# Optimization experiments

Measured on AMD Instinct MI355X. Metric: run time of the kernel, lower is better.

The kernel has to match this reference:

```python
import jax, jax.numpy as jnp
import numpy as np

EPS_LN = 1e-5
EPS_BN = 1e-5
NUM_HEADS = 8


def _gelu(x):
    return jax.nn.gelu(x, approximate=False)


def _ln(x, w, b):
    # LayerNorm over last (channel) dim, eps=1e-5 (torch default)
    mu = jnp.mean(x, axis=-1, keepdims=True)
    var = jnp.mean((x - mu) ** 2, axis=-1, keepdims=True)
    return (x - mu) / jnp.sqrt(var + EPS_LN) * w + b


def _bn(x, g, b):
    # eval-mode BatchNorm2d on NCHW with running_mean=0, running_var=1
    scale = g * (1.0 + EPS_BN) ** -0.5
    return x * scale[None, :, None, None] + b[None, :, None, None]


def _conv1x1(x, w):
    # x: [B,C,H,W], w: [O,C]
    return jnp.einsum('bchw,oc->bohw', x, w)


def _unfold3(x, r):
    # nn.Unfold(kernel=3, dilation=r, padding=r): gather 3x3 dilated neighborhoods
    B, C, H, W = x.shape
    xp = jnp.pad(x, ((0, 0), (0, 0), (r, r), (r, r)))
    pats = [xp[:, :, i * r:i * r + H, j * r:j * r + W] for i in range(3) for j in range(3)]
    return jnp.stack(pats, axis=2)  # [B,C,9,H,W]


def _atrous_attn(q, k, v, num_heads, r):
    # per-pixel local attention: q [B,C,H,W] attends to 9 dilated neighbors of k/v
    B, C, H, W = q.shape
    hd = C // num_heads
    scale = hd ** -0.5
    qh = q.reshape(B, num_heads, hd, H, W)
    kp = _unfold3(k, r).reshape(B, num_heads, hd, 9, H, W)
    attn = jax.nn.softmax(jnp.einsum('bnchw,bnckhw->bnkhw', qh, kp) * scale, axis=2)
    vp = _unfold3(v, r).reshape(B, num_heads, hd, 9, H, W)
    out = jnp.einsum('bnkhw,bnckhw->bnchw', attn, vp)
    return out.reshape(B, C, H, W).transpose(0, 2, 3, 1)  # [B,H,W,C]


def _window_attn(x_bhwc, qkv_w, proj_w, proj_b, num_heads, r):
    xc = x_bhwc.transpose(0, 3, 1, 2)
    C = xc.shape[1]
    qkv = _conv1x1(xc, qkv_w)  # [B,3C,H,W], order q|k|v
    out = _atrous_attn(qkv[:, :C], qkv[:, C:2 * C], qkv[:, 2 * C:], num_heads, r)
    return jnp.einsum('bhwc,oc->bhwo', out, proj_w) + proj_b


def _mlp(x_bhwc, c1_w, c1_b, bn1_g, bn1_b, dw_w, dw_b, bn2_g, bn2_b, c2_w, c2_b, bn3_g, bn3_b):
    xc = x_bhwc.transpose(0, 3, 1, 2)
    h = _bn(_gelu(_conv1x1(xc, c1_w) + c1_b[None, :, None, None]), bn1_g, bn1_b)
    dw = jax.lax.conv_general_dilated(h, dw_w, (1, 1), 'SAME',
                                      feature_group_count=h.shape[1],
                                      dimension_numbers=('NCHW', 'OIHW', 'NCHW'))
    dw = dw + dw_b[None, :, None, None]
    h = _bn(_gelu(dw + h), bn2_g, bn2_b)
    out = _bn(_conv1x1(h, c2_w) + c2_b[None, :, None, None], bn3_g, bn3_b)
    return out.transpose(0, 2, 3, 1)


def reference(x, ln1_w, ln1_b, ln2_w, ln2_b,
              qkv1_w, proj1_w, proj1_b, qkv2_w, proj2_w, proj2_b, qkv3_w, proj3_w, proj3_b,
              tc_conv_w, tc_conv_b, tc_bn1_g, tc_bn1_b, tc_pool_w, tc_bn2_g, tc_bn2_b,
              tc_trans_w, tc_trans_b, tc_bn3_g, tc_bn3_b,
              mlp_c1_w, mlp_c1_b, mlp_bn1_g, mlp_bn1_b, mlp_dw_w, mlp_dw_b,
              mlp_bn2_g, mlp_bn2_b, mlp_c2_w, mlp_c2_b, mlp_bn3_g, mlp_bn3_b):
    tx = x.transpose(0, 2, 3, 1)  # [B,H,W,C]
    n1 = _ln(tx, ln1_w, ln1_b)
    t1 = tx + _window_attn(n1, qkv1_w, proj1_w, proj1_b, NUM_HEADS, 1)
    t2 = tx + _window_attn(n1, qkv2_w, proj2_w, proj2_b, NUM_HEADS, 2)
    t3 = tx + _window_attn(n1, qkv3_w, proj3_w, proj3_b, NUM_HEADS, 3)
    # Trans_conv: ASPP-style fusion
    xc1 = jax.nn.relu(_bn(_conv1x1(x, tc_conv_w) + tc_conv_b[None, :, None, None], tc_bn1_g, tc_bn1_b))
    pool = jnp.mean(x, axis=(2, 3), keepdims=True)
    pool = jax.nn.relu(_bn(_conv1x1(pool, tc_pool_w), tc_bn2_g, tc_bn2_b))
    pool = jnp.broadcast_to(pool, x.shape)  # bilinear upsample of a 1x1 map == broadcast
    cat = jnp.concatenate([xc1, t1.transpose(0, 3, 1, 2), t2.transpose(0, 3, 1, 2),
                           t3.transpose(0, 3, 1, 2), pool], axis=1)  # [B,5C,H,W]
    tr = jax.nn.relu(_bn(_conv1x1(cat, tc_trans_w) + tc_trans_b[None, :, None, None],
                         tc_bn3_g, tc_bn3_b)).transpose(0, 2, 3, 1)  # [B,H,W,C]
    tr = tr + _mlp(_ln(tr, ln2_w, ln2_b), mlp_c1_w, mlp_c1_b, mlp_bn1_g, mlp_bn1_b,
                   mlp_dw_w, mlp_dw_b, mlp_bn2_g, mlp_bn2_b, mlp_c2_w, mlp_c2_b,
                   mlp_bn3_g, mlp_bn3_b)
    return tr.transpose(0, 3, 1, 2)  # [B,C,H,W]


def setup_inputs():
    key = jax.random.key(0)
    B, C, H, W = 4, 256, 64, 64
    HID = 4 * C
    ks = iter(jax.random.split(key, 64))

    def nrm(shape, scale=0.02):
        return jax.random.normal(next(ks), shape, dtype=jnp.float32) * scale

    inp = {
        'x': jax.random.normal(next(ks), (B, C, H, W), dtype=jnp.float32),
        'ln1_w': jnp.ones((C,), jnp.float32), 'ln1_b': jnp.zeros((C,), jnp.float32),
        'ln2_w': jnp.ones((C,), jnp.float32), 'ln2_b': jnp.zeros((C,), jnp.float32),
    }
    for i in (1, 2, 3):
        inp[f'qkv{i}_w'] = nrm((3 * C, C))
        inp[f'proj{i}_w'] = nrm((C, C))
        inp[f'proj{i}_b'] = jnp.zeros((C,), jnp.float32)
    inp.update(
        tc_conv_w=nrm((C, C)), tc_conv_b=jnp.zeros((C,), jnp.float32),
        tc_bn1_g=jnp.ones((C,), jnp.float32), tc_bn1_b=jnp.zeros((C,), jnp.float32),
        tc_pool_w=nrm((C, C)),
        tc_bn2_g=jnp.ones((C,), jnp.float32), tc_bn2_b=jnp.zeros((C,), jnp.float32),
        tc_trans_w=nrm((C, 5 * C)), tc_trans_b=jnp.zeros((C,), jnp.float32),
        tc_bn3_g=jnp.ones((C,), jnp.float32), tc_bn3_b=jnp.zeros((C,), jnp.float32),
        mlp_c1_w=nrm((HID, C)), mlp_c1_b=jnp.zeros((HID,), jnp.float32),
        mlp_bn1_g=jnp.ones((HID,), jnp.float32), mlp_bn1_b=jnp.zeros((HID,), jnp.float32),
        mlp_dw_w=nrm((HID, 1, 3, 3), 0.1), mlp_dw_b=jnp.zeros((HID,), jnp.float32),
        mlp_bn2_g=jnp.ones((HID,), jnp.float32), mlp_bn2_b=jnp.zeros((HID,), jnp.float32),
        mlp_c2_w=nrm((C, HID)), mlp_c2_b=jnp.zeros((C,), jnp.float32),
        mlp_bn3_g=jnp.ones((C,), jnp.float32), mlp_bn3_b=jnp.zeros((C,), jnp.float32),
    )
    return inp
```

## Files before the change

kernel.cpp:

```cpp
#include <hip/hip_runtime.h>

#define N_PIX 16384
#define CDIM  256
#define HIDD  1024
#define BNS   0.9999950000374997f

typedef __attribute__((ext_vector_type(8))) short  short8;
typedef __attribute__((ext_vector_type(4))) float  f32x4;
typedef __attribute__((ext_vector_type(4))) int    int4v;
typedef __attribute__((ext_vector_type(2))) int    int2v;

__device__ __forceinline__ float b2f(unsigned short u){
  unsigned int x = ((unsigned int)u) << 16; float f;
  __builtin_memcpy(&f, &x, 4); return f;
}
__device__ __forceinline__ unsigned short f2b(float f){
  unsigned int x; __builtin_memcpy(&x, &f, 4);
  unsigned int r = (x + 0x7fffu + ((x >> 16) & 1u)) >> 16;
  return (unsigned short)r;
}
__device__ __forceinline__ float geluf(float x){
  return 0.5f * x * (1.0f + erff(x * 0.70710678118654752f));
}

typedef const __attribute__((address_space(1))) unsigned int* gas_t;
typedef __attribute__((address_space(3))) unsigned int*       las_t;
__device__ __forceinline__ void gload16(const void* g, void* l){
  __builtin_amdgcn_global_load_lds((gas_t)g, (las_t)l, 16, 0, 0);
}

__global__ __launch_bounds__(256) void k_cvt_all(
    const float* __restrict__ s0, const float* __restrict__ s1, const float* __restrict__ s2,
    const float* __restrict__ s3, const float* __restrict__ s4, const float* __restrict__ s5,
    const float* __restrict__ s6, const float* __restrict__ s7, const float* __restrict__ s8,
    const float* __restrict__ s9, unsigned short* __restrict__ wb){
  const float* srcs[10] = {s0,s1,s2,s3,s4,s5,s6,s7,s8,s9};
  const int n[10]   = {196608,196608,196608,65536,65536,65536,65536,327680,262144,262144};
  const int off[10] = {0,196608,393216,589824,655360,720896,786432,851968,1179648,1441792};
  int seg = blockIdx.y;
  int i = (blockIdx.x * 256 + threadIdx.x) * 8;
  if (i >= n[seg]) return;
  const float* src = srcs[seg];
  unsigned short* dst = wb + off[seg];
  f32x4 a = *(const f32x4*)(src + i);
  f32x4 b = *(const f32x4*)(src + i + 4);
  unsigned short o[8];
  #pragma unroll
  for (int j = 0; j < 4; ++j){ o[j] = f2b(a[j]); o[4 + j] = f2b(b[j]); }
  *(int4v*)(dst + i) = *(int4v*)o;
}

__global__ __launch_bounds__(256) void k_dwwT(const float* __restrict__ dww,
                                              unsigned short* __restrict__ dwwT,
                                              float* __restrict__ pm){
  int i = blockIdx.x * 256 + threadIdx.x;
  if (i < 1024) pm[i] = 0.0f;
  if (i >= 9216) return;
  int kk = i >> 10, c = i & 1023;
  dwwT[i] = f2b(dww[c * 9 + kk]);
}

__global__ __launch_bounds__(256) void k_transpose(const float* __restrict__ x,
                                                   unsigned short* __restrict__ xpm,
                                                   float* __restrict__ xpm32,
                                                   float* __restrict__ pm){
  __shared__ __align__(16) float tile[64][65];
  int b = blockIdx.z, c0 = blockIdx.y * 64, p0 = blockIdx.x * 64;
  int t = threadIdx.x;
  int r = t >> 3, k = t & 7;
  float psum[2];
  for (int s = 0; s < 2; ++s){
    int rr = r + s * 32;
    const float* src = x + (((size_t)(b * CDIM + c0 + rr)) << 12) + p0 + k * 8;
    f32x4 a = *(const f32x4*)src;
    f32x4 c = *(const f32x4*)(src + 4);
    psum[s] = a[0] + a[1] + a[2] + a[3] + c[0] + c[1] + c[2] + c[3];
    #pragma unroll
    for (int j = 0; j < 4; ++j){ tile[rr][k * 8 + j] = a[j]; tile[rr][k * 8 + 4 + j] = c[j]; }
  }
  #pragma unroll
  for (int s = 0; s < 2; ++s){
    float v = psum[s];
    v += __shfl_xor(v, 1); v += __shfl_xor(v, 2); v += __shfl_xor(v, 4);
    if ((t & 7) == 0) atomicAdd(&pm[b * 256 + c0 + r + s * 32], v);
  }
  __syncthreads();
  for (int s = 0; s < 2; ++s){
    int pr = r + s * 32;
    float tf[8];
    unsigned short tb[8];
    #pragma unroll
    for (int j = 0; j < 8; ++j){ tf[j] = tile[k * 8 + j][pr]; tb[j] = f2b(tf[j]); }
    size_t rowoff = ((size_t)(b * 4096 + p0 + pr)) << 8;
    *(int4v*)(xpm + rowoff + c0 + k * 8) = *(int4v*)tb;
    *(f32x4*)(xpm32 + rowoff + c0 + k * 8)     = *(f32x4*)&tf[0];
    *(f32x4*)(xpm32 + rowoff + c0 + k * 8 + 4) = *(f32x4*)&tf[4];
  }
}

template<typename IT>
__global__ __launch_bounds__(256) void k_ln(const IT* __restrict__ in,
    const float* __restrict__ w, const float* __restrict__ bia,
    unsigned short* __restrict__ out){
  int row  = blockIdx.x * 4 + (threadIdx.x >> 6);
  int lane = threadIdx.x & 63;
  float v[4];
  const IT* p = in + (size_t)row * CDIM + lane * 4;
  if constexpr (sizeof(IT) == 2){
    int2v d = *(const int2v*)p;
    unsigned short tmp[4]; __builtin_memcpy(tmp, &d, 8);
    #pragma unroll
    for (int j = 0; j < 4; ++j) v[j] = b2f(tmp[j]);
  } else {
    f32x4 d = *(const f32x4*)p;
    #pragma unroll
    for (int j = 0; j < 4; ++j) v[j] = d[j];
  }
  float s  = v[0] + v[1] + v[2] + v[3];
  float s2 = v[0]*v[0] + v[1]*v[1] + v[2]*v[2] + v[3]*v[3];
  #pragma unroll
  for (int m = 1; m < 64; m <<= 1){
    s  += __shfl_xor(s,  m);
    s2 += __shfl_xor(s2, m);
  }
  float mu   = s * (1.0f / 256.0f);
  float var  = s2 * (1.0f / 256.0f) - mu * mu;
  float rstd = rsqrtf(var + 1e-5f);
  unsigned short o[4];
  #pragma unroll
  for (int j = 0; j < 4; ++j){
    int c = lane * 4 + j;
    o[j] = f2b((v[j] - mu) * rstd * w[c] + bia[c]);
  }
  *(int2v*)(out + (size_t)row * CDIM + lane * 4) = *(int2v*)o;
}

template<int MODE, int BM>
__global__ __launch_bounds__(256) void k_gemm(
    const unsigned short* __restrict__ A, const unsigned short* __restrict__ Bw,
    int K, int Nout, int ldb, void* __restrict__ outp,
    const float* __restrict__ bias,
    const float* __restrict__ bng,
    const float* __restrict__ bnb,
    const float* __restrict__ auxf,
    int catoff)
{
  constexpr int NI = BM / 32;
  __shared__ __align__(16) unsigned short As[2][BM * 32];
  __shared__ __align__(16) unsigned short Bs[2][128 * 32];
  int t = threadIdx.x;
  int m0 = blockIdx.y * BM, n0 = blockIdx.x * 128;
  int lane = t & 63;
  int w  = __builtin_amdgcn_readfirstlane(t >> 6);
  int wm = w >> 1, wn = w & 1;
  int lr = lane & 15, kb = lane >> 4;
  const bool doA = (w * 16 < BM);

  f32x4 acc[NI][4];
  f32x4 z = {0.f, 0.f, 0.f, 0.f};
  #pragma unroll
  for (int i = 0; i < NI; ++i)
    #pragma unroll
    for (int j = 0; j < 4; ++j) acc[i][j] = z;

  int srow = lane >> 2;
  int schunk = (((lane & 3) ^ ((lane >> 3) & 3))) * 8;
  const unsigned short* gA  = A  + (size_t)(m0 + w * 16 + srow) * K   + schunk;
  const unsigned short* gB0 = Bw + (size_t)(n0 + w * 16 + srow) * ldb + schunk;
  const unsigned short* gB1 = Bw + (size_t)(n0 + 64 + w * 16 + srow) * ldb + schunk;
  int kbx = (kb ^ ((lr >> 1) & 3)) * 8;

  const int nt = K >> 5;
  if (doA) gload16(gA, As[0] + w * 512);
  gload16(gB0, Bs[0] + w * 512);
  gload16(gB1, Bs[0] + 2048 + w * 512);

  for (int tt = 0; tt < nt; ++tt){
    int cur = tt & 1;
    if (tt + 1 < nt){
      int k1 = (tt + 1) << 5;
      if (doA) gload16(gA + k1, As[cur ^ 1] + w * 512);
      gload16(gB0 + k1, Bs[cur ^ 1] + w * 512);
      gload16(gB1 + k1, Bs[cur ^ 1] + 2048 + w * 512);
      if (doA) asm volatile("s_waitcnt vmcnt(3)" ::: "memory");
      else     asm volatile("s_waitcnt vmcnt(2)" ::: "memory");
    } else {
      asm volatile("s_waitcnt vmcnt(0)" ::: "memory");
    }
    __builtin_amdgcn_s_barrier();
    short8 af[NI], bf_[4];
    #pragma unroll
    for (int i = 0; i < NI; ++i)
      af [i] = *(const short8*)&As[cur][(wm * (BM / 2) + i * 16 + lr) * 32 + kbx];
    #pragma unroll
    for (int j = 0; j < 4; ++j)
      bf_[j] = *(const short8*)&Bs[cur][(wn * 64 + j * 16 + lr) * 32 + kbx];
    #pragma unroll
    for (int i = 0; i < NI; ++i)
      #pragma unroll
      for (int j = 0; j < 4; ++j)
        acc[i][j] = __builtin_amdgcn_mfma_f32_16x16x32_bf16(af[i], bf_[j], acc[i][j], 0, 0, 0);
    asm volatile("s_waitcnt lgkmcnt(0)" ::: "memory");
    __builtin_amdgcn_sched_barrier(0);
    __builtin_amdgcn_s_barrier();
  }

  #pragma unroll
  for (int i = 0; i < NI; ++i){
    int rowb = m0 + wm * (BM / 2) + i * 16 + kb * 4;
    #pragma unroll
    for (int j = 0; j < 4; ++j){
      int col = n0 + wn * 64 + j * 16 + lr;
      #pragma unroll
      for (int rr = 0; rr < 4; ++rr){
        int row = rowb + rr;
        float v = acc[i][j][rr];
        if constexpr (MODE == 0){
          ((unsigned short*)outp)[(size_t)row * Nout + col] = f2b(v);
        } else if constexpr (MODE == 3){
          v += bias[col] + auxf[((row >> 12) << 8) + col];
          v = v * (bng[col] * BNS) + bnb[col];
          v = fmaxf(v, 0.0f);
          ((float*)outp)[(size_t)row * CDIM + col] = v;
        } else if constexpr (MODE == 4){
          v = geluf(v + bias[col]);
          v = v * (bng[col] * BNS) + bnb[col];
          ((unsigned short*)outp)[(size_t)row * HIDD + col] = f2b(v);
        } else {
          v = (v + bias[col]) * (bng[col] * BNS) + bnb[col];
          v += auxf[(size_t)row * CDIM + col];
          int b = row >> 12, hw = row & 4095;
          ((float*)outp)[(((size_t)(b * CDIM + col)) << 12) + hw] = v;
        }
      }
    }
  }
}

struct GrpArgs {
  const unsigned short* A[4];
  const unsigned short* B[4];
  const float* bias[4];
  int lda[4];
  int catoff[4];
};

__global__ __launch_bounds__(256) void k_gemm_grp(GrpArgs ga,
    const float* __restrict__ xpm32, const float* __restrict__ bng,
    const float* __restrict__ bnb, unsigned short* __restrict__ CAT)
{
  __shared__ __align__(16) unsigned short As[2][64 * 32];
  __shared__ __align__(16) unsigned short Bs[2][128 * 32];
  int t = threadIdx.x;
  int g  = blockIdx.x >> 1;
  int n0 = (blockIdx.x & 1) * 128;
  int m0 = blockIdx.y * 64;
  const unsigned short* A  = ga.A[g];
  const unsigned short* Bw = ga.B[g];
  const float* bias = ga.bias[g];
  int lda = ga.lda[g];
  int catoff = ga.catoff[g];

  int lane = t & 63;
  int w  = __builtin_amdgcn_readfirstlane(t >> 6);
  int wm = w >> 1, wn = w & 1;
  int lr = lane & 15, kb = lane >> 4;

  f32x4 acc[2][4];
  f32x4 z = {0.f, 0.f, 0.f, 0.f};
  #pragma unroll
  for (int i = 0; i < 2; ++i)
    #pragma unroll
    for (int j = 0; j < 4; ++j) acc[i][j] = z;

  int srow = lane >> 2;
  int schunk = (((lane & 3) ^ ((lane >> 3) & 3))) * 8;
  const unsigned short* gA  = A  + (size_t)(m0 + w * 16 + srow) * lda + schunk;
  const unsigned short* gB0 = Bw + (size_t)(n0 + w * 16 + srow) * 256 + schunk;
  const unsigned short* gB1 = Bw + (size_t)(n0 + 64 + w * 16 + srow) * 256 + schunk;
  int kbx = (kb ^ ((lr >> 1) & 3)) * 8;

  gload16(gA,  As[0] + w * 512);
  gload16(gB0, Bs[0] + w * 512);
  gload16(gB1, Bs[0] + 2048 + w * 512);

  for (int tt = 0; tt < 8; ++tt){
    int cur = tt & 1;
    if (tt + 1 < 8){
      int k1 = (tt + 1) << 5;
      gload16(gA  + k1, As[cur ^ 1] + w * 512);
      gload16(gB0 + k1, Bs[cur ^ 1] + w * 512);
      gload16(gB1 + k1, Bs[cur ^ 1] + 2048 + w * 512);
      asm volatile("s_waitcnt vmcnt(3)" ::: "memory");
    } else {
      asm volatile("s_waitcnt vmcnt(0)" ::: "memory");
    }
    __builtin_amdgcn_s_barrier();
    short8 af[2], bf_[4];
    #pragma unroll
    for (int i = 0; i < 2; ++i)
      af [i] = *(const short8*)&As[cur][(wm * 32 + i * 16 + lr) * 32 + kbx];
    #pragma unroll
    for (int j = 0; j < 4; ++j)
      bf_[j] = *(const short8*)&Bs[cur][(wn * 64 + j * 16 + lr) * 32 + kbx];
    #pragma unroll
    for (int i = 0; i < 2; ++i)
      #pragma unroll
      for (int j = 0; j < 4; ++j)
        acc[i][j] = __builtin_amdgcn_mfma_f32_16x16x32_bf16(af[i], bf_[j], acc[i][j], 0, 0, 0);
    asm volatile("s_waitcnt lgkmcnt(0)" ::: "memory");
    __builtin_amdgcn_sched_barrier(0);
    __builtin_amdgcn_s_barrier();
  }

  #pragma unroll
  for (int i = 0; i < 2; ++i){
    int rowb = m0 + wm * 32 + i * 16 + kb * 4;
    #pragma unroll
    for (int j = 0; j < 4; ++j){
      int col = n0 + wn * 64 + j * 16 + lr;
      #pragma unroll
      for (int rr = 0; rr < 4; ++rr){
        int row = rowb + rr;
        float v = acc[i][j][rr];
        if (g == 3){
          v = (v + bias[col]) * (bng[col] * BNS) + bnb[col];
          v = fmaxf(v, 0.0f);
        } else {
          v += bias[col] + xpm32[(size_t)row * CDIM + col];
        }
        CAT[(size_t)row * HIDD + catoff + col] = f2b(v);
      }
    }
  }
}

__global__ __launch_bounds__(256) void k_attn3(const unsigned short* __restrict__ QKV3,
                                               unsigned short* __restrict__ F3){
  int grp = blockIdx.x >> 10;
  int r = grp + 1;
  int t = (blockIdx.x & 1023) * 256 + threadIdx.x;
  int half = t & 1, head = (t >> 1) & 7, pix = t >> 4;
  int hw = pix & 4095, h = hw >> 6, w = hw & 63;
  const unsigned short* base = QKV3 + (size_t)pix * 2304 + grp * 768 + head * 32 + half * 16;

  float q[16];
  #pragma unroll
  for (int c8 = 0; c8 < 2; ++c8){
    int4v d = *(const int4v*)(base + c8 * 8);
    unsigned short tmp[8]; __builtin_memcpy(tmp, &d, 16);
    #pragma unroll
    for (int j = 0; j < 8; ++j) q[c8 * 8 + j] = b2f(tmp[j]);
  }
  float logit[9];
  #pragma unroll
  for (int jj = 0; jj < 9; ++jj){
    int dh = (jj / 3 - 1) * r, dw = (jj % 3 - 1) * r;
    int hh = h + dh, ww = w + dw;
    float d = 0.0f;
    if (hh >= 0 && hh < 64 && ww >= 0 && ww < 64){
      const unsigned short* kr = base + (dh * 64 + dw) * 2304 + 256;
      #pragma unroll
      for (int c8 = 0; c8 < 2; ++c8){
        int4v dd = *(const int4v*)(kr + c8 * 8);
        unsigned short tmp[8]; __builtin_memcpy(tmp, &dd, 16);
        #pragma unroll
        for (int j = 0; j < 8; ++j) d += q[c8 * 8 + j] * b2f(tmp[j]);
      }
    }
    d += __shfl_xor(d, 1);
    logit[jj] = d * 0.17677669529663687f;
  }
  float m = logit[0];
  #pragma unroll
  for (int jj = 1; jj < 9; ++jj) m = fmaxf(m, logit[jj]);
  float p[9], s = 0.0f;
  #pragma unroll
  for (int jj = 0; jj < 9; ++jj){ p[jj] = __expf(logit[jj] - m); s += p[jj]; }
  float inv = 1.0f / s;
  float o[16];
  #pragma unroll
  for (int j = 0; j < 16; ++j) o[j] = 0.0f;
  #pragma unroll
  for (int jj = 0; jj < 9; ++jj){
    int dh = (jj / 3 - 1) * r, dw = (jj % 3 - 1) * r;
    int hh = h + dh, ww = w + dw;
    if (hh >= 0 && hh < 64 && ww >= 0 && ww < 64){
      float pj = p[jj] * inv;
      const unsigned short* vr = base + (dh * 64 + dw) * 2304 + 512;
      #pragma unroll
      for (int c8 = 0; c8 < 2; ++c8){
        int4v dd = *(const int4v*)(vr + c8 * 8);
        unsigned short tmp[8]; __builtin_memcpy(tmp, &dd, 16);
        #pragma unroll
        for (int j = 0; j < 8; ++j) o[c8 * 8 + j] += pj * b2f(tmp[j]);
      }
    }
  }
  unsigned short ob[16];
  #pragma unroll
  for (int j = 0; j < 16; ++j) ob[j] = f2b(o[j]);
  unsigned short* op = F3 + (size_t)pix * 768 + grp * 256 + head * 32 + half * 16;
  *(int4v*)(op)     = *(int4v*)&ob[0];
  *(int4v*)(op + 8) = *(int4v*)&ob[8];
}

__global__ __launch_bounds__(256) void k_dwconv(const unsigned short* __restrict__ H,
    const unsigned short* __restrict__ dwwT, const float* __restrict__ dwb,
    const float* __restrict__ g, const float* __restrict__ bb,
    unsigned short* __restrict__ H2){
  int t = blockIdx.x * 256 + threadIdx.x;
  int chunk = t & 127, pix = t >> 7;
  int hw = pix & 4095, h = hw >> 6, w = hw & 63;
  int c0 = chunk * 8;
  float acc[8], hc[8];
  {
    int4v dd = *(const int4v*)(H + (size_t)pix * HIDD + c0);
    unsigned short tmp[8]; __builtin_memcpy(tmp, &dd, 16);
    #pragma unroll
    for (int j = 0; j < 8; ++j){ hc[j] = b2f(tmp[j]); acc[j] = 0.0f; }
  }
  #pragma unroll
  for (int di = -1; di <= 1; ++di)
    #pragma unroll
    for (int dj = -1; dj <= 1; ++dj){
      int hh = h + di, ww = w + dj;
      if (hh < 0 || hh >= 64 || ww < 0 || ww >= 64) continue;
      int kk = (di + 1) * 3 + (dj + 1);
      int4v dd = *(const int4v*)(H + ((size_t)(pix + di * 64 + dj)) * HIDD + c0);
      int4v wv = *(const int4v*)(dwwT + kk * 1024 + c0);
      unsigned short tmp[8], wt[8];
      __builtin_memcpy(tmp, &dd, 16);
      __builtin_memcpy(wt,  &wv, 16);
      #pragma unroll
      for (int j = 0; j < 8; ++j) acc[j] += b2f(wt[j]) * b2f(tmp[j]);
    }
  f32x4 bv0 = *(const f32x4*)(dwb + c0), bv1 = *(const f32x4*)(dwb + c0 + 4);
  f32x4 gv0 = *(const f32x4*)(g   + c0), gv1 = *(const f32x4*)(g   + c0 + 4);
  f32x4 cv0 = *(const f32x4*)(bb  + c0), cv1 = *(const f32x4*)(bb  + c0 + 4);
  float bvv[8], gvv[8], cvv[8];
  #pragma unroll
  for (int j = 0; j < 4; ++j){
    bvv[j] = bv0[j]; bvv[4 + j] = bv1[j];
    gvv[j] = gv0[j]; gvv[4 + j] = gv1[j];
    cvv[j] = cv0[j]; cvv[4 + j] = cv1[j];
  }
  unsigned short ob[8];
  #pragma unroll
  for (int j = 0; j < 8; ++j){
    float v = acc[j] + bvv[j] + hc[j];
    v = geluf(v);
    v = v * (gvv[j] * BNS) + cvv[j];
    ob[j] = f2b(v);
  }
  *(int4v*)(H2 + (size_t)pix * HIDD + c0) = *(int4v*)ob;
}

__global__ __launch_bounds__(256) void k_poolfb(const float* __restrict__ pm,
    const float* __restrict__ pw, const float* __restrict__ g,
    const float* __restrict__ bb, const float* __restrict__ tw,
    float* __restrict__ pb){
  int b = blockIdx.x, o = threadIdx.x;
  __shared__ float v[256];
  __shared__ float pfs[256];
  v[o] = pm[b * 256 + o] * (1.0f / 4096.0f);
  __syncthreads();
  float acc = 0.0f;
  const float* wr = pw + (size_t)o * 256;
  for (int c = 0; c < 256; ++c) acc += v[c] * wr[c];
  float val = acc * (g[o] * BNS) + bb[o];
  pfs[o] = fmaxf(val, 0.0f);
  __syncthreads();
  float acc2 = 0.0f;
  const float* tr = tw + (size_t)o * 1280 + 1024;
  for (int c = 0; c < 256; ++c) acc2 += pfs[c] * tr[c];
  pb[b * 256 + o] = acc2;
}

extern "C" void kernel_launch(void* const* d_in, const int* in_sizes, int n_in,
                              void* d_out, int out_size, void* d_ws, size_t ws_size,
                              hipStream_t stream){
  const float* x     = (const float*)d_in[0];
  const float* ln1w  = (const float*)d_in[1];
  const float* ln1b  = (const float*)d_in[2];
  const float* ln2w  = (const float*)d_in[3];
  const float* ln2b  = (const float*)d_in[4];
  const float* qkvw[3]  = {(const float*)d_in[5], (const float*)d_in[8],  (const float*)d_in[11]};
  const float* projw[3] = {(const float*)d_in[6], (const float*)d_in[9],  (const float*)d_in[12]};
  const float* projb[3] = {(const float*)d_in[7], (const float*)d_in[10], (const float*)d_in[13]};
  const float* tcw   = (const float*)d_in[14];
  const float* tcb   = (const float*)d_in[15];
  const float* bn1g  = (const float*)d_in[16];
  const float* bn1b  = (const float*)d_in[17];
  const float* poolw = (const float*)d_in[18];
  const float* bn2g  = (const float*)d_in[19];
  const float* bn2b  = (const float*)d_in[20];
  const float* trw   = (const float*)d_in[21];
  const float* trb   = (const float*)d_in[22];
  const float* bn3g  = (const float*)d_in[23];
  const float* bn3b  = (const float*)d_in[24];
  const float* c1w   = (const float*)d_in[25];
  const float* c1b   = (const float*)d_in[26];
  const float* mbn1g = (const float*)d_in[27];
  const float* mbn1b = (const float*)d_in[28];
  const float* dww   = (const float*)d_in[29];
  const float* dwb   = (const float*)d_in[30];
  const float* mbn2g = (const float*)d_in[31];
  const float* mbn2b = (const float*)d_in[32];
  const float* c2w   = (const float*)d_in[33];
  const float* c2b   = (const float*)d_in[34];
  const float* mbn3g = (const float*)d_in[35];
  const float* mbn3b = (const float*)d_in[36];

  char* ws = (char*)d_ws;
  unsigned short* Xpm = (unsigned short*)(ws);
  unsigned short* N1  = (unsigned short*)(ws + 8388608);
  unsigned short* CAT = (unsigned short*)(ws + 16777216);
  float*          TR  = (float*)        (ws + 50331648);
  float*          Xpm32 = TR;
  unsigned short* H   = (unsigned short*)(ws + 67108864);
  unsigned short* H2  = (unsigned short*)(ws + 100663296);
  unsigned short* Wb  = (unsigned short*)(ws + 134217728);
  unsigned short* projbw[3] = {Wb + 589824, Wb + 655360, Wb + 720896};
  unsigned short* tcwb  = Wb + 786432;
  unsigned short* trwb  = Wb + 851968;
  unsigned short* c1wb  = Wb + 1179648;
  unsigned short* c2wb  = Wb + 1441792;
  unsigned short* dwwT  = Wb + 1703936;
  float*          pm  = (float*)(ws + 134217728 + 3428352);
  float*          pb  = pm + 1024;
  unsigned short* E3  = (unsigned short*)(ws + 140509184);
  unsigned short* F3  = (unsigned short*)(ws + 216006656);

  k_cvt_all<<<dim3(160, 10), 256, 0, stream>>>(qkvw[0], qkvw[1], qkvw[2],
                                               projw[0], projw[1], projw[2],
                                               tcw, trw, c1w, c2w, Wb);
  k_dwwT<<<36, 256, 0, stream>>>(dww, dwwT, pm);
  k_transpose<<<dim3(64, 4, 4), 256, 0, stream>>>(x, Xpm, Xpm32, pm);
  k_ln<unsigned short><<<4096, 256, 0, stream>>>(Xpm, ln1w, ln1b, N1);
  k_poolfb<<<4, 256, 0, stream>>>(pm, poolw, bn2g, bn2b, trw, pb);

  k_gemm<0, 64><<<dim3(18, 256), 256, 0, stream>>>(N1, Wb, 256, 2304, 256, E3,
                                                   nullptr, nullptr, nullptr, nullptr, 0);
  k_attn3<<<3072, 256, 0, stream>>>(E3, F3);
  {
    GrpArgs ga;
    ga.A[0] = F3;       ga.A[1] = F3 + 256; ga.A[2] = F3 + 512; ga.A[3] = Xpm;
    ga.B[0] = projbw[0]; ga.B[1] = projbw[1]; ga.B[2] = projbw[2]; ga.B[3] = tcwb;
    ga.bias[0] = projb[0]; ga.bias[1] = projb[1]; ga.bias[2] = projb[2]; ga.bias[3] = tcb;
    ga.lda[0] = 768; ga.lda[1] = 768; ga.lda[2] = 768; ga.lda[3] = 256;
    ga.catoff[0] = 256; ga.catoff[1] = 512; ga.catoff[2] = 768; ga.catoff[3] = 0;
    k_gemm_grp<<<dim3(8, 256), 256, 0, stream>>>(ga, Xpm32, bn1g, bn1b, CAT);
  }
  k_gemm<3, 32><<<dim3(2, 512), 256, 0, stream>>>(CAT, trwb, 1024, 256, 1280, TR,
                                                  trb, bn3g, bn3b, pb, 0);
  k_ln<float><<<4096, 256, 0, stream>>>(TR, ln2w, ln2b, N1);
  k_gemm<4, 64><<<dim3(8, 256), 256, 0, stream>>>(N1, c1wb, 256, 1024, 256, H,
                                                  c1b, mbn1g, mbn1b, nullptr, 0);
  k_dwconv<<<8192, 256, 0, stream>>>(H, dwwT, dwb, mbn2g, mbn2b, H2);
  k_gemm<5, 32><<<dim3(2, 512), 256, 0, stream>>>(H2, c2wb, 1024, 256, 1024, d_out,
                                                  c2b, mbn3g, mbn3b, TR, 0);
}
```

Measured before the change: 398.3 us.

## Triple-buffer LDS tiles in GEMM kernels to prefetch two stages ahead

```diff
diff --git a/kernel.cpp b/kernel.cpp
--- a/kernel.cpp
+++ b/kernel.cpp
@@ -146,8 +146,8 @@
     int catoff)
 {
   constexpr int NI = BM / 32;
-  __shared__ __align__(16) unsigned short As[2][BM * 32];
-  __shared__ __align__(16) unsigned short Bs[2][128 * 32];
+  __shared__ __align__(16) unsigned short As[3][BM * 32];
+  __shared__ __align__(16) unsigned short Bs[3][128 * 32];
   int t = threadIdx.x;
   int m0 = blockIdx.y * BM, n0 = blockIdx.x * 128;
   int lane = t & 63;
@@ -174,18 +174,28 @@
   if (doA) gload16(gA, As[0] + w * 512);
   gload16(gB0, Bs[0] + w * 512);
   gload16(gB1, Bs[0] + 2048 + w * 512);
-
+  if (doA) gload16(gA + 32, As[1] + w * 512);
+  gload16(gB0 + 32, Bs[1] + w * 512);
+  gload16(gB1 + 32, Bs[1] + 2048 + w * 512);
+
+  int cur = 0;
   for (int tt = 0; tt < nt; ++tt){
-    int cur = tt & 1;
-    if (tt + 1 < nt){
-      int k1 = (tt + 1) << 5;
-      if (doA) gload16(gA + k1, As[cur ^ 1] + w * 512);
-      gload16(gB0 + k1, Bs[cur ^ 1] + w * 512);
-      gload16(gB1 + k1, Bs[cur ^ 1] + 2048 + w * 512);
-      if (doA) asm volatile("s_waitcnt vmcnt(3)" ::: "memory");
-      else     asm volatile("s_waitcnt vmcnt(2)" ::: "memory");
+    if (tt + 2 < nt){
+      int k2 = (tt + 2) << 5;
+      int nxt = cur + 2; if (nxt >= 3) nxt -= 3;
+      if (doA) gload16(gA + k2, As[nxt] + w * 512);
+      gload16(gB0 + k2, Bs[nxt] + w * 512);
+      gload16(gB1 + k2, Bs[nxt] + 2048 + w * 512);
+    }
+    int ahead = nt - 1 - tt; if (ahead > 2) ahead = 2;
+    if (doA){
+      if (ahead == 2)      asm volatile("s_waitcnt vmcnt(6)" ::: "memory");
+      else if (ahead == 1) asm volatile("s_waitcnt vmcnt(3)" ::: "memory");
+      else                 asm volatile("s_waitcnt vmcnt(0)" ::: "memory");
     } else {
-      asm volatile("s_waitcnt vmcnt(0)" ::: "memory");
+      if (ahead == 2)      asm volatile("s_waitcnt vmcnt(4)" ::: "memory");
+      else if (ahead == 1) asm volatile("s_waitcnt vmcnt(2)" ::: "memory");
+      else                 asm volatile("s_waitcnt vmcnt(0)" ::: "memory");
     }
     __builtin_amdgcn_s_barrier();
     short8 af[NI], bf_[4];
@@ -203,6 +213,7 @@
     asm volatile("s_waitcnt lgkmcnt(0)" ::: "memory");
     __builtin_amdgcn_sched_barrier(0);
     __builtin_amdgcn_s_barrier();
+    ++cur; if (cur >= 3) cur = 0;
   }
 
   #pragma unroll
@@ -249,8 +260,8 @@
     const float* __restrict__ xpm32, const float* __restrict__ bng,
     const float* __restrict__ bnb, unsigned short* __restrict__ CAT)
 {
-  __shared__ __align__(16) unsigned short As[2][64 * 32];
-  __shared__ __align__(16) unsigned short Bs[2][128 * 32];
+  __shared__ __align__(16) unsigned short As[3][64 * 32];
+  __shared__ __align__(16) unsigned short Bs[3][128 * 32];
   int t = threadIdx.x;
   int g  = blockIdx.x >> 1;
   int n0 = (blockIdx.x & 1) * 128;
@@ -283,18 +294,23 @@
   gload16(gA,  As[0] + w * 512);
   gload16(gB0, Bs[0] + w * 512);
   gload16(gB1, Bs[0] + 2048 + w * 512);
-
+  gload16(gA + 32,  As[1] + w * 512);
+  gload16(gB0 + 32, Bs[1] + w * 512);
+  gload16(gB1 + 32, Bs[1] + 2048 + w * 512);
+
+  int cur = 0;
   for (int tt = 0; tt < 8; ++tt){
-    int cur = tt & 1;
-    if (tt + 1 < 8){
-      int k1 = (tt + 1) << 5;
-      gload16(gA  + k1, As[cur ^ 1] + w * 512);
-      gload16(gB0 + k1, Bs[cur ^ 1] + w * 512);
-      gload16(gB1 + k1, Bs[cur ^ 1] + 2048 + w * 512);
-      asm volatile("s_waitcnt vmcnt(3)" ::: "memory");
-    } else {
-      asm volatile("s_waitcnt vmcnt(0)" ::: "memory");
-    }
+    if (tt + 2 < 8){
+      int k2 = (tt + 2) << 5;
+      int nxt = cur + 2; if (nxt >= 3) nxt -= 3;
+      gload16(gA  + k2, As[nxt] + w * 512);
+      gload16(gB0 + k2, Bs[nxt] + w * 512);
+      gload16(gB1 + k2, Bs[nxt] + 2048 + w * 512);
+    }
+    int ahead = 7 - tt; if (ahead > 2) ahead = 2;
+    if (ahead == 2)      asm volatile("s_waitcnt vmcnt(6)" ::: "memory");
+    else if (ahead == 1) asm volatile("s_waitcnt vmcnt(3)" ::: "memory");
+    else                 asm volatile("s_waitcnt vmcnt(0)" ::: "memory");
     __builtin_amdgcn_s_barrier();
     short8 af[2], bf_[4];
     #pragma unroll
@@ -311,6 +327,7 @@
     asm volatile("s_waitcnt lgkmcnt(0)" ::: "memory");
     __builtin_amdgcn_sched_barrier(0);
     __builtin_amdgcn_s_barrier();
+    ++cur; if (cur >= 3) cur = 0;
   }
 
   #pragma unroll
```

After: 402.6 us. About the same (+1.1%).
